# Performance work log

Measured on AMD Instinct MI355X. Metric: run time of the kernel, lower is better.

The kernel has to match this reference:

```python
import jax, jax.numpy as jnp
import numpy as np

B, S, D = 16, 256, 256      # batch, seq_len, input_size (= 2*hidden)
H = 128                     # hidden size per direction
NL = 2                      # num layers
A = 8                       # n_actions
DK = D // 4                 # attention projection dim = 64
SRU_IN = 2 * D              # cat(rnn_input, attn_pool) = 512


def setup_inputs() -> dict:
    key = jax.random.key(0)
    ks = jax.random.split(key, 12)
    stdv = 1.0 / np.sqrt(DK)
    inp = {
        "x": jax.random.normal(ks[0], (B, S, D), jnp.float32),
        "x_mask": jnp.zeros((B, S), bool),
        "actions": jax.random.randint(ks[1], (B,), 0, A),
        # SeqAttentionAction params (reset_parameters: uniform(-stdv,stdv), biases zero)
        "w1": jax.random.uniform(ks[2], (A, D, DK), jnp.float32, -stdv, stdv),
        "b1": jnp.zeros((A, DK), jnp.float32),
        "w2": jax.random.uniform(ks[3], (A, D, DK), jnp.float32, -stdv, stdv),
        "b2": jnp.zeros((A, DK), jnp.float32),
        "v": jax.random.uniform(ks[4], (A, DK), jnp.float32, -stdv, stdv),
        # SRU params: per layer, forward & backward cells. k=4 slices (x~, f, r, highway)
        "sru_w_f": jax.random.uniform(ks[5], (NL, SRU_IN, 4 * H), jnp.float32, -0.05, 0.05),
        "sru_b_f": jnp.zeros((NL, 2 * H), jnp.float32),
        "sru_w_b": jax.random.uniform(ks[6], (NL, SRU_IN, 4 * H), jnp.float32, -0.05, 0.05),
        "sru_b_b": jnp.zeros((NL, 2 * H), jnp.float32),
    }
    return inp


def _sru_layer(X, W, b):
    """SRU (use_tanh=1). X:(S,B,Din) -> (S,B,H)."""
    U = jnp.einsum("sbd,dk->sbk", X, W)           # (S,B,4H)
    u0, uf, ur, hw = jnp.split(U, 4, axis=-1)
    bf, br = jnp.split(b, 2)
    f = jax.nn.sigmoid(uf + bf)
    r = jax.nn.sigmoid(ur + br)

    def step(c, t):
        f_t, u_t, r_t, hw_t = t
        c = f_t * c + (1.0 - f_t) * u_t
        h = r_t * jnp.tanh(c) + (1.0 - r_t) * hw_t
        return c, h

    c0 = jnp.zeros((X.shape[1], f.shape[-1]), X.dtype)
    _, hs = jax.lax.scan(step, c0, (f, u0, r, hw))
    return hs


def _attn_pools(memory, rnn_input, x_mask, w1a, b1a, w2a, b2a, va):
    """Action-conditioned tanh attention, vectorized over all timesteps.
    memory:(B,L,D) rnn_input:(S,B,D) -> pools:(S,B,D) (detached, as in torch .data)."""
    xt = jnp.einsum("bld,bdk->blk", memory, w1a) + b1a[:, None]    # (B,L,K)
    yt = jnp.einsum("sbd,bdk->sbk", rnn_input, w2a) + b2a[None]    # (S,B,K)
    t = jnp.tanh(xt[None] + yt[:, :, None])                        # (S,B,L,K)
    scores = jnp.einsum("sblk,bk->sbl", t, va)                     # (S,B,L)
    scores = jnp.where(x_mask[None], -jnp.inf, scores)
    att = jax.nn.softmax(scores, axis=-1)
    pools = jnp.einsum("sbl,bld->sbd", att, memory)
    return jax.lax.stop_gradient(pools)


def reference(x, x_mask, actions, w1, b1, w2, b2, v,
              sru_w_f, sru_b_f, sru_w_b, sru_b_b):
    memory = x                                # (B,L,D)
    out = jnp.transpose(x, (1, 0, 2))         # (S,B,D)
    # one-hot matmul selection == gather by action index
    w1a, b1a = w1[actions], b1[actions]
    w2a, b2a = w2[actions], b2[actions]
    va = v[actions]
    for i in range(NL):
        pools = _attn_pools(memory, out, x_mask, w1a, b1a, w2a, b2a, va)
        inputs = jnp.concatenate([out, pools], axis=2)   # (S,B,2D); inputs_f == inputs_b
        hf = _sru_layer(inputs, sru_w_f[i], sru_b_f[i])
        hb = _sru_layer(inputs, sru_w_b[i], sru_b_b[i])
        out = jnp.concatenate([hf, hb], axis=2)          # (S,B,2H)=(S,B,D)
    return jnp.transpose(out, (1, 0, 2))                 # (B,S,D)
```

## Files before the change

kernel.cpp:

```cpp
#include <hip/hip_runtime.h>
#include <hip/hip_bf16.h>

#define S_ 256
#define D_ 256
#define K_ 64
#define SIN 512
#define F4H 512

typedef unsigned short u16;
typedef __attribute__((ext_vector_type(8))) short short8;
typedef __attribute__((ext_vector_type(4))) float f32x4;

__device__ __forceinline__ float rcpf(float x) { return __builtin_amdgcn_rcpf(x); }
__device__ __forceinline__ float fast_sigmoid(float x) {
  return rcpf(1.0f + __expf(-x));
}
__device__ __forceinline__ float fast_tanh(float x) {
  return 1.0f - 2.0f * rcpf(__expf(2.0f * x) + 1.0f);
}
__device__ __forceinline__ u16 f2bf(float f) {
  unsigned int u = __float_as_uint(f);
  return (u16)((u + 0x7fff + ((u >> 16) & 1)) >> 16);
}

__global__ __launch_bounds__(256) void k_prep(const float* __restrict__ sw_f,
    const float* __restrict__ sw_b, u16* __restrict__ wt,
    const float* __restrict__ x, u16* __restrict__ xT,
    const int* __restrict__ araw, int* __restrict__ act_out,
    int* __restrict__ status) {
  if (blockIdx.x == 0 && blockIdx.y == 0 && blockIdx.z == 0 && threadIdx.x == 0) {
    bool oddzero = true;
    for (int i = 1; i < 16; i += 2) oddzero = oddzero && (araw[i] == 0);
    bool ok = true;
    for (int b = 0; b < 16; ++b) {
      int v = oddzero ? araw[2 * b] : araw[b];
      act_out[b] = (v < 0) ? 0 : (v > 7 ? 7 : v);
      ok = ok && (v >= 0 && v < 8);
    }
    *status = ok ? 1 : 0;
  }
  __shared__ u16 tile[64][66];
  int tj = threadIdx.x & 63, ti = threadIdx.x >> 6;
  int z = blockIdx.z;
  if (z < 4) {
    int layer = z >> 1;
    const float* src = (z & 1) ? sw_b : sw_f;
    int k0 = blockIdx.x * 64, n0 = blockIdx.y * 64;
#pragma unroll
    for (int i = ti; i < 64; i += 4)
      tile[i][tj] = f2bf(src[layer * 262144 + (k0 + i) * 512 + n0 + tj]);
    __syncthreads();
#pragma unroll
    for (int j = ti; j < 64; j += 4)
      wt[z * 262144 + (n0 + j) * 512 + k0 + tj] = tile[tj][j];
  } else {
    if (blockIdx.x >= 4 || blockIdx.y >= 4) return;
    int b = z - 4;
    int l0 = blockIdx.x * 64, d0 = blockIdx.y * 64;
#pragma unroll
    for (int i = ti; i < 64; i += 4)
      tile[i][tj] = f2bf(x[b * 65536 + (l0 + i) * 256 + d0 + tj]);
    __syncthreads();
#pragma unroll
    for (int j = ti; j < 64; j += 4)
      xT[b * 65536 + (d0 + j) * 256 + l0 + tj] = tile[tj][j];
  }
}

__global__ __launch_bounds__(256) void k_xt(const float* __restrict__ x,
    const int* __restrict__ act, const float* __restrict__ w1,
    const float* __restrict__ b1, float* __restrict__ xtT) {
  __shared__ float As[16][17], Bs[16][68];
  int b = blockIdx.y;
  int a = act[b];
  int l0 = blockIdx.x * 16;
  const float* A = x + b * (S_ * D_);
  const float* W = w1 + a * (D_ * K_);
  int tid = threadIdx.x;
  int ty = tid >> 4, tx = tid & 15;
  float acc[4] = {};
  for (int kk = 0; kk < D_; kk += 16) {
    As[ty][tx] = A[(l0 + ty) * D_ + kk + tx];
    *(float4*)&Bs[ty][tx << 2] = *(const float4*)(W + (kk + ty) * K_ + (tx << 2));
    __syncthreads();
#pragma unroll
    for (int k = 0; k < 16; ++k) {
      float av = As[ty][k];
      acc[0] += av * Bs[k][(tx << 2) + 0];
      acc[1] += av * Bs[k][(tx << 2) + 1];
      acc[2] += av * Bs[k][(tx << 2) + 2];
      acc[3] += av * Bs[k][(tx << 2) + 3];
    }
    __syncthreads();
  }
#pragma unroll
  for (int j = 0; j < 4; ++j) {
    int n = (tx << 2) + j;
    xtT[(b << 14) + n * 256 + l0 + ty] = acc[j] + b1[a * K_ + n];
  }
}

__global__ __launch_bounds__(256) void k_score(const float* __restrict__ xtT,
    const float* __restrict__ curb, int sstride, int bstride,
    const float* __restrict__ w2, const float* __restrict__ b2,
    const float* __restrict__ v, const int* __restrict__ act,
    const unsigned char* __restrict__ xmask, u16* __restrict__ scores) {
  __shared__ float yts[4][K_], vas[K_], curs[4][256];
  __shared__ float redm[4][4], reds[4][4];
  int tid = threadIdx.x;
  int bid = blockIdx.x;
  int b = bid & 15, s4 = bid >> 4;
  int a = act[b];
  if (tid < 64) vas[tid] = v[a * K_ + tid];
#pragma unroll
  for (int rr = 0; rr < 4; ++rr)
    curs[rr][tid] = curb[b * bstride + (s4 * 4 + rr) * sstride + tid];
  __syncthreads();
  {
    int r = tid >> 6, k = tid & 63;
    const float* wcol = w2 + a * (D_ * K_) + k;
    float accv = b2[a * K_ + k];
#pragma unroll 8
    for (int d = 0; d < 256; ++d) accv += curs[r][d] * wcol[d * K_];
    yts[r][k] = accv;
  }
  __syncthreads();
  float acc0 = 0.f, acc1 = 0.f, acc2 = 0.f, acc3 = 0.f;
  {
    const float* xb = xtT + (b << 14) + tid;
#pragma unroll
    for (int k = 0; k < 64; ++k) {
      float xv = xb[k * 256];
      float vv = vas[k];
      acc0 += vv * fast_tanh(xv + yts[0][k]);
      acc1 += vv * fast_tanh(xv + yts[1][k]);
      acc2 += vv * fast_tanh(xv + yts[2][k]);
      acc3 += vv * fast_tanh(xv + yts[3][k]);
    }
    if (xmask[b * S_ + tid]) { acc0 = acc1 = acc2 = acc3 = -1e30f; }
  }
  int wid = tid >> 6;
  float m0 = acc0, m1 = acc1, m2 = acc2, m3 = acc3;
#pragma unroll
  for (int d = 32; d; d >>= 1) {
    m0 = fmaxf(m0, __shfl_xor(m0, d));
    m1 = fmaxf(m1, __shfl_xor(m1, d));
    m2 = fmaxf(m2, __shfl_xor(m2, d));
    m3 = fmaxf(m3, __shfl_xor(m3, d));
  }
  if ((tid & 63) == 0) {
    redm[0][wid] = m0; redm[1][wid] = m1; redm[2][wid] = m2; redm[3][wid] = m3;
  }
  __syncthreads();
  m0 = fmaxf(fmaxf(redm[0][0], redm[0][1]), fmaxf(redm[0][2], redm[0][3]));
  m1 = fmaxf(fmaxf(redm[1][0], redm[1][1]), fmaxf(redm[1][2], redm[1][3]));
  m2 = fmaxf(fmaxf(redm[2][0], redm[2][1]), fmaxf(redm[2][2], redm[2][3]));
  m3 = fmaxf(fmaxf(redm[3][0], redm[3][1]), fmaxf(redm[3][2], redm[3][3]));
  float p0 = __expf(acc0 - m0), p1 = __expf(acc1 - m1);
  float p2 = __expf(acc2 - m2), p3 = __expf(acc3 - m3);
  float s0 = p0, s1 = p1, s2 = p2, s3 = p3;
#pragma unroll
  for (int d = 32; d; d >>= 1) {
    s0 += __shfl_xor(s0, d);
    s1 += __shfl_xor(s1, d);
    s2 += __shfl_xor(s2, d);
    s3 += __shfl_xor(s3, d);
  }
  if ((tid & 63) == 0) {
    reds[0][wid] = s0; reds[1][wid] = s1; reds[2][wid] = s2; reds[3][wid] = s3;
  }
  __syncthreads();
  s0 = reds[0][0] + reds[0][1] + reds[0][2] + reds[0][3];
  s1 = reds[1][0] + reds[1][1] + reds[1][2] + reds[1][3];
  s2 = reds[2][0] + reds[2][1] + reds[2][2] + reds[2][3];
  s3 = reds[3][0] + reds[3][1] + reds[3][2] + reds[3][3];
  u16* dst = scores + ((s4 * 4) * 16 + b) * 256 + tid;
  dst[0]        = f2bf(p0 * rcpf(s0));
  dst[16 * 256] = f2bf(p1 * rcpf(s1));
  dst[32 * 256] = f2bf(p2 * rcpf(s2));
  dst[48 * 256] = f2bf(p3 * rcpf(s3));
}

__global__ __launch_bounds__(256) void k_poolm(const u16* __restrict__ scores,
    const u16* __restrict__ xT, const float* __restrict__ curb,
    int sstride, int bstride, u16* __restrict__ inp) {
  __shared__ u16 As[128][72];
  __shared__ u16 Bs[128][72];
  int b = blockIdx.z;
  int m0 = blockIdx.x * 128, n0 = blockIdx.y * 128;
  int tid = threadIdx.x;
  int wid = tid >> 6, lane = tid & 63;
  int wm = wid >> 1, wn = wid & 1;
  f32x4 acc[4][4];
#pragma unroll
  for (int i = 0; i < 4; ++i)
#pragma unroll
    for (int j = 0; j < 4; ++j) acc[i][j] = (f32x4){0.f, 0.f, 0.f, 0.f};
  int srow = tid >> 1, shalf = tid & 1;
  int lrow = lane & 15, lk = (lane >> 4) << 3;
  for (int kk = 0; kk < 256; kk += 64) {
    const u16* ga = scores + ((m0 + srow) * 16 + b) * 256 + kk + shalf * 32;
    const u16* gb = xT + b * 65536 + (n0 + srow) * 256 + kk + shalf * 32;
#pragma unroll
    for (int j = 0; j < 4; ++j) {
      *(short8*)&As[srow][shalf * 32 + j * 8] = *(const short8*)(ga + j * 8);
      *(short8*)&Bs[srow][shalf * 32 + j * 8] = *(const short8*)(gb + j * 8);
    }
    __syncthreads();
#pragma unroll
    for (int ks = 0; ks < 2; ++ks) {
      short8 af[4], bf[4];
#pragma unroll
      for (int mi = 0; mi < 4; ++mi)
        af[mi] = *(const short8*)&As[wm * 64 + mi * 16 + lrow][ks * 32 + lk];
#pragma unroll
      for (int ni = 0; ni < 4; ++ni)
        bf[ni] = *(const short8*)&Bs[wn * 64 + ni * 16 + lrow][ks * 32 + lk];
#pragma unroll
      for (int mi = 0; mi < 4; ++mi)
#pragma unroll
        for (int ni = 0; ni < 4; ++ni)
          acc[mi][ni] = __builtin_amdgcn_mfma_f32_16x16x32_bf16(
              af[mi], bf[ni], acc[mi][ni], 0, 0, 0);
    }
    __syncthreads();
  }
#pragma unroll
  for (int mi = 0; mi < 4; ++mi)
#pragma unroll
    for (int ni = 0; ni < 4; ++ni) {
      int r0 = m0 + wm * 64 + mi * 16 + ((lane >> 4) << 2);
      int c = n0 + wn * 64 + ni * 16 + (lane & 15);
#pragma unroll
      for (int r = 0; r < 4; ++r)
        inp[((r0 + r) * 16 + b) * SIN + 256 + c] = f2bf(acc[mi][ni][r]);
    }
#pragma unroll
  for (int i = 0; i < 16; ++i) {
    int idx = i * 256 + tid;
    int so = idx >> 5, d4 = (idx & 31) << 2;
    float4 v4 = *(const float4*)(curb + b * bstride + (m0 + so) * sstride + n0 + d4);
    ushort4 o;
    o.x = f2bf(v4.x); o.y = f2bf(v4.y); o.z = f2bf(v4.z); o.w = f2bf(v4.w);
    *(ushort4*)(inp + ((m0 + so) * 16 + b) * SIN + n0 + d4) = o;
  }
}

__global__ __launch_bounds__(256) void k_mfma(const u16* __restrict__ inp,
    const u16* __restrict__ wt, float* __restrict__ Uf, float* __restrict__ Ub,
    int layer) {
  __shared__ u16 As[128][72];
  __shared__ u16 Bs[128][72];
  float* U = blockIdx.z ? Ub : Uf;
  const u16* W = wt + (layer * 2 + blockIdx.z) * 262144;
  int m0 = blockIdx.x * 128, n0 = blockIdx.y * 128;
  int tid = threadIdx.x;
  int wid = tid >> 6, lane = tid & 63;
  int wm = wid >> 1, wn = wid & 1;
  f32x4 acc[4][4];
#pragma unroll
  for (int i = 0; i < 4; ++i)
#pragma unroll
    for (int j = 0; j < 4; ++j) acc[i][j] = (f32x4){0.f, 0.f, 0.f, 0.f};
  int srow = tid >> 1, shalf = tid & 1;
  int lrow = lane & 15, lk = (lane >> 4) << 3;
  for (int kk = 0; kk < 512; kk += 64) {
    const u16* ga = inp + (m0 + srow) * SIN + kk + shalf * 32;
    const u16* gb = W + (n0 + srow) * 512 + kk + shalf * 32;
#pragma unroll
    for (int j = 0; j < 4; ++j) {
      *(short8*)&As[srow][shalf * 32 + j * 8] = *(const short8*)(ga + j * 8);
      *(short8*)&Bs[srow][shalf * 32 + j * 8] = *(const short8*)(gb + j * 8);
    }
    __syncthreads();
#pragma unroll
    for (int ks = 0; ks < 2; ++ks) {
      short8 af[4], bf[4];
#pragma unroll
      for (int mi = 0; mi < 4; ++mi)
        af[mi] = *(const short8*)&As[wm * 64 + mi * 16 + lrow][ks * 32 + lk];
#pragma unroll
      for (int ni = 0; ni < 4; ++ni)
        bf[ni] = *(const short8*)&Bs[wn * 64 + ni * 16 + lrow][ks * 32 + lk];
#pragma unroll
      for (int mi = 0; mi < 4; ++mi)
#pragma unroll
        for (int ni = 0; ni < 4; ++ni)
          acc[mi][ni] = __builtin_amdgcn_mfma_f32_16x16x32_bf16(
              af[mi], bf[ni], acc[mi][ni], 0, 0, 0);
    }
    __syncthreads();
  }
#pragma unroll
  for (int mi = 0; mi < 4; ++mi)
#pragma unroll
    for (int ni = 0; ni < 4; ++ni) {
      int r0 = m0 + wm * 64 + mi * 16 + ((lane >> 4) << 2);
      int c = n0 + wn * 64 + ni * 16 + (lane & 15);
#pragma unroll
      for (int r = 0; r < 4; ++r)
        U[(r0 + r) * F4H + c] = acc[mi][ni][r];
    }
}

__global__ __launch_bounds__(256) void k_scan(const float* __restrict__ Uf,
    const float* __restrict__ Ub, const float* __restrict__ bfp,
    const float* __restrict__ bbp, float* __restrict__ obase,
    int o_sstride, int o_bstride, const int* __restrict__ status, int final) {
  int tid = threadIdx.x;
  int chain = blockIdx.x * 16 + (tid >> 4);
  int lane = tid & 15;
  int dir = chain >> 11;
  int rem = chain & 2047;
  int b = rem >> 7, h = rem & 127;
  const float* U = dir ? Ub : Uf;
  const float* bias = dir ? bbp : bfp;
  float bfv = bias[h], brv = bias[128 + h];
  const float* up = U + b * 512 + h;
  float* op = obase + b * o_bstride + dir * 128 + h;
  int s0 = lane * 16;
  float fv[16], u0[16], rv[16], hw[16];
#pragma unroll
  for (int t = 0; t < 16; ++t) {
    const float* q = up + (s0 + t) * 8192;
    u0[t] = q[0]; fv[t] = q[128]; rv[t] = q[256]; hw[t] = q[384];
  }
  float A = 1.f, Bv = 0.f;
#pragma unroll
  for (int t = 0; t < 16; ++t) {
    float f = fast_sigmoid(fv[t] + bfv);
    fv[t] = f;
    Bv = f * Bv + (1.f - f) * u0[t];
    A = A * f;
  }
#pragma unroll
  for (int d = 1; d < 16; d <<= 1) {
    float Ap = __shfl_up(A, d, 16);
    float Bp = __shfl_up(Bv, d, 16);
    if (lane >= d) { Bv = A * Bp + Bv; A = A * Ap; }
  }
  float cin = __shfl_up(Bv, 1, 16);
  if (lane == 0) cin = 0.f;
  float c = cin;
  bool ok = final ? (*status != 0) : true;
#pragma unroll
  for (int t = 0; t < 16; ++t) {
    float f = fv[t];
    c = f * (c - u0[t]) + u0[t];
    float r = fast_sigmoid(rv[t] + brv);
    float hv = r * fast_tanh(c) + (1.f - r) * hw[t];
    op[(s0 + t) * o_sstride] = ok ? hv : 20.0f;
  }
}

__global__ __launch_bounds__(256) void k_fill(float* out, float v, int n) {
  int idx = blockIdx.x * 256 + threadIdx.x;
  if (idx < n) out[idx] = v;
}

extern "C" void kernel_launch(void* const* d_in, const int* in_sizes, int n_in,
                              void* d_out, int out_size, void* d_ws, size_t ws_size,
                              hipStream_t stream) {
  float* out = (float*)d_out;
  int fill_grid = (out_size + 255) / 256;

  const int exp_sizes[12] = {1048576, 4096, 16, 131072, 512, 131072, 512, 512,
                             524288, 512, 524288, 512};
  bool env_ok = (n_in == 12);
  if (env_ok)
    for (int i = 0; i < 12; ++i) env_ok = env_ok && (in_sizes[i] == exp_sizes[i]);
  if (!env_ok) {
    k_fill<<<fill_grid, 256, 0, stream>>>(out, 10.0f, out_size);
    return;
  }

  const float* x    = (const float*)d_in[0];
  const unsigned char* xmask = (const unsigned char*)d_in[1];
  const float* w1   = (const float*)d_in[3];
  const float* b1   = (const float*)d_in[4];
  const float* w2   = (const float*)d_in[5];
  const float* b2   = (const float*)d_in[6];
  const float* v    = (const float*)d_in[7];
  const float* sw_f = (const float*)d_in[8];
  const float* sb_f = (const float*)d_in[9];
  const float* sw_b = (const float*)d_in[10];
  const float* sb_b = (const float*)d_in[11];

  float* ws = (float*)d_ws;
  size_t off = 0;
  float* pb0    = ws + off; off += 1048576;
  float* xtT    = ws + off; off += 262144;
  float* Uf     = ws + off; off += 2097152;
  float* Ub     = ws + off; off += 2097152;
  u16*   scores = (u16*)(ws + off); off += 524288;
  u16*   xT     = (u16*)(ws + off); off += 524288;
  u16*   inp    = (u16*)(ws + off); off += 1048576;
  u16*   wt     = (u16*)(ws + off); off += 524288;
  int*   act    = (int*)(ws + off); off += 16;
  int*   status = (int*)(ws + off); off += 16;

  if (ws_size < off * sizeof(float)) {
    k_fill<<<fill_grid, 256, 0, stream>>>(out, 30.0f, out_size);
    return;
  }

  k_prep<<<dim3(8, 8, 20), 256, 0, stream>>>(sw_f, sw_b, wt, x, xT,
      (const int*)d_in[2], act, status);
  k_xt<<<dim3(16, 16), 256, 0, stream>>>(x, act, w1, b1, xtT);

  for (int layer = 0; layer < 2; ++layer) {
    const float* curb = layer ? pb0 : x;
    int sstride = layer ? 4096 : 256;
    int bstride = layer ? 256 : 65536;
    float* nxt      = layer ? out : pb0;
    int o_sstride   = layer ? 256 : 4096;
    int o_bstride   = layer ? 65536 : 256;
    k_score<<<1024, 256, 0, stream>>>(xtT, curb, sstride, bstride, w2, b2, v,
                                      act, xmask, scores);
    k_poolm<<<dim3(2, 2, 16), 256, 0, stream>>>(scores, xT, curb, sstride,
                                                bstride, inp);
    k_mfma<<<dim3(32, 4, 2), 256, 0, stream>>>(inp, wt, Uf, Ub, layer);
    k_scan<<<256, 256, 0, stream>>>(Uf, Ub, sb_f + layer * 256, sb_b + layer * 256,
                                    nxt, o_sstride, o_bstride, status, layer);
  }
}
```

Before: 166.2 us.

## Split yt projection into tiled kernel, shrink pool tiles, stage scan output via LDS

Moves the per-timestep w2 projection out of k_score into a separate shared-memory tiled GEMM kernel, so w2 columns are no longer reloaded per block with strided access. It also halves the k_poolm tile to 64x64 so the grid grows from 64 to 256 blocks, and stages k_scan outputs in LDS so global writes are coalesced along h instead of strided. The cost is one extra kernel launch per layer and an extra workspace buffer round-trip.

Result: faster. 156.4 us (-5.9%).

```diff
diff --git a/kernel.cpp b/kernel.cpp
--- a/kernel.cpp
+++ b/kernel.cpp
@@ -100,29 +100,55 @@
   }
 }
 
+__global__ __launch_bounds__(256) void k_yt(const float* __restrict__ curb,
+    int sstride, int bstride, const int* __restrict__ act,
+    const float* __restrict__ w2, const float* __restrict__ b2,
+    float* __restrict__ yt) {
+  __shared__ float As[16][17], Bs[16][68];
+  int b = blockIdx.y;
+  int a = act[b];
+  int s0 = blockIdx.x * 16;
+  const float* A = curb + b * bstride;
+  const float* W = w2 + a * (D_ * K_);
+  int tid = threadIdx.x;
+  int ty = tid >> 4, tx = tid & 15;
+  float acc[4] = {};
+  for (int kk = 0; kk < D_; kk += 16) {
+    As[ty][tx] = A[(s0 + ty) * sstride + kk + tx];
+    *(float4*)&Bs[ty][tx << 2] = *(const float4*)(W + (kk + ty) * K_ + (tx << 2));
+    __syncthreads();
+#pragma unroll
+    for (int k = 0; k < 16; ++k) {
+      float av = As[ty][k];
+      acc[0] += av * Bs[k][(tx << 2) + 0];
+      acc[1] += av * Bs[k][(tx << 2) + 1];
+      acc[2] += av * Bs[k][(tx << 2) + 2];
+      acc[3] += av * Bs[k][(tx << 2) + 3];
+    }
+    __syncthreads();
+  }
+  float4 o;
+  o.x = acc[0] + b2[a * K_ + (tx << 2) + 0];
+  o.y = acc[1] + b2[a * K_ + (tx << 2) + 1];
+  o.z = acc[2] + b2[a * K_ + (tx << 2) + 2];
+  o.w = acc[3] + b2[a * K_ + (tx << 2) + 3];
+  *(float4*)(yt + ((s0 + ty) * 16 + b) * K_ + (tx << 2)) = o;
+}
+
 __global__ __launch_bounds__(256) void k_score(const float* __restrict__ xtT,
-    const float* __restrict__ curb, int sstride, int bstride,
-    const float* __restrict__ w2, const float* __restrict__ b2,
-    const float* __restrict__ v, const int* __restrict__ act,
-    const unsigned char* __restrict__ xmask, u16* __restrict__ scores) {
-  __shared__ float yts[4][K_], vas[K_], curs[4][256];
+    const float* __restrict__ yt, const float* __restrict__ v,
+    const int* __restrict__ act, const unsigned char* __restrict__ xmask,
+    u16* __restrict__ scores) {
+  __shared__ float yts[4][K_], vas[K_];
   __shared__ float redm[4][4], reds[4][4];
   int tid = threadIdx.x;
   int bid = blockIdx.x;
   int b = bid & 15, s4 = bid >> 4;
   int a = act[b];
   if (tid < 64) vas[tid] = v[a * K_ + tid];
-#pragma unroll
-  for (int rr = 0; rr < 4; ++rr)
-    curs[rr][tid] = curb[b * bstride + (s4 * 4 + rr) * sstride + tid];
-  __syncthreads();
   {
-    int r = tid >> 6, k = tid & 63;
-    const float* wcol = w2 + a * (D_ * K_) + k;
-    float accv = b2[a * K_ + k];
-#pragma unroll 8
-    for (int d = 0; d < 256; ++d) accv += curs[r][d] * wcol[d * K_];
-    yts[r][k] = accv;
+    int row = tid >> 6, k = tid & 63;
+    yts[row][k] = yt[((s4 * 4 + row) * 16 + b) * K_ + k];
   }
   __syncthreads();
   float acc0 = 0.f, acc1 = 0.f, acc2 = 0.f, acc3 = 0.f;
@@ -184,61 +210,60 @@
 __global__ __launch_bounds__(256) void k_poolm(const u16* __restrict__ scores,
     const u16* __restrict__ xT, const float* __restrict__ curb,
     int sstride, int bstride, u16* __restrict__ inp) {
-  __shared__ u16 As[128][72];
-  __shared__ u16 Bs[128][72];
+  __shared__ u16 As[64][72];
+  __shared__ u16 Bs[64][72];
   int b = blockIdx.z;
-  int m0 = blockIdx.x * 128, n0 = blockIdx.y * 128;
+  int m0 = blockIdx.x * 64, n0 = blockIdx.y * 64;
   int tid = threadIdx.x;
   int wid = tid >> 6, lane = tid & 63;
   int wm = wid >> 1, wn = wid & 1;
-  f32x4 acc[4][4];
-#pragma unroll
-  for (int i = 0; i < 4; ++i)
-#pragma unroll
-    for (int j = 0; j < 4; ++j) acc[i][j] = (f32x4){0.f, 0.f, 0.f, 0.f};
-  int srow = tid >> 1, shalf = tid & 1;
+  f32x4 acc[2][2];
+#pragma unroll
+  for (int i = 0; i < 2; ++i)
+#pragma unroll
+    for (int j = 0; j < 2; ++j) acc[i][j] = (f32x4){0.f, 0.f, 0.f, 0.f};
+  int srow = tid >> 2, soff = (tid & 3) * 16;
   int lrow = lane & 15, lk = (lane >> 4) << 3;
   for (int kk = 0; kk < 256; kk += 64) {
-    const u16* ga = scores + ((m0 + srow) * 16 + b) * 256 + kk + shalf * 32;
-    const u16* gb = xT + b * 65536 + (n0 + srow) * 256 + kk + shalf * 32;
-#pragma unroll
-    for (int j = 0; j < 4; ++j) {
-      *(short8*)&As[srow][shalf * 32 + j * 8] = *(const short8*)(ga + j * 8);
-      *(short8*)&Bs[srow][shalf * 32 + j * 8] = *(const short8*)(gb + j * 8);
-    }
+    const u16* ga = scores + ((m0 + srow) * 16 + b) * 256 + kk + soff;
+    const u16* gb = xT + b * 65536 + (n0 + srow) * 256 + kk + soff;
+    *(short8*)&As[srow][soff]     = *(const short8*)(ga);
+    *(short8*)&As[srow][soff + 8] = *(const short8*)(ga + 8);
+    *(short8*)&Bs[srow][soff]     = *(const short8*)(gb);
+    *(short8*)&Bs[srow][soff + 8] = *(const short8*)(gb + 8);
     __syncthreads();
 #pragma unroll
     for (int ks = 0; ks < 2; ++ks) {
-      short8 af[4], bf[4];
-#pragma unroll
-      for (int mi = 0; mi < 4; ++mi)
-        af[mi] = *(const short8*)&As[wm * 64 + mi * 16 + lrow][ks * 32 + lk];
-#pragma unroll
-      for (int ni = 0; ni < 4; ++ni)
-        bf[ni] = *(const short8*)&Bs[wn * 64 + ni * 16 + lrow][ks * 32 + lk];
-#pragma unroll
-      for (int mi = 0; mi < 4; ++mi)
-#pragma unroll
-        for (int ni = 0; ni < 4; ++ni)
+      short8 af[2], bf[2];
+#pragma unroll
+      for (int mi = 0; mi < 2; ++mi)
+        af[mi] = *(const short8*)&As[wm * 32 + mi * 16 + lrow][ks * 32 + lk];
+#pragma unroll
+      for (int ni = 0; ni < 2; ++ni)
+        bf[ni] = *(const short8*)&Bs[wn * 32 + ni * 16 + lrow][ks * 32 + lk];
+#pragma unroll
+      for (int mi = 0; mi < 2; ++mi)
+#pragma unroll
+        for (int ni = 0; ni < 2; ++ni)
           acc[mi][ni] = __builtin_amdgcn_mfma_f32_16x16x32_bf16(
               af[mi], bf[ni], acc[mi][ni], 0, 0, 0);
     }
     __syncthreads();
   }
 #pragma unroll
-  for (int mi = 0; mi < 4; ++mi)
-#pragma unroll
-    for (int ni = 0; ni < 4; ++ni) {
-      int r0 = m0 + wm * 64 + mi * 16 + ((lane >> 4) << 2);
-      int c = n0 + wn * 64 + ni * 16 + (lane & 15);
+  for (int mi = 0; mi < 2; ++mi)
+#pragma unroll
+    for (int ni = 0; ni < 2; ++ni) {
+      int r0 = m0 + wm * 32 + mi * 16 + ((lane >> 4) << 2);
+      int c = n0 + wn * 32 + ni * 16 + (lane & 15);
 #pragma unroll
       for (int r = 0; r < 4; ++r)
         inp[((r0 + r) * 16 + b) * SIN + 256 + c] = f2bf(acc[mi][ni][r]);
     }
 #pragma unroll
-  for (int i = 0; i < 16; ++i) {
+  for (int i = 0; i < 4; ++i) {
     int idx = i * 256 + tid;
-    int so = idx >> 5, d4 = (idx & 31) << 2;
+    int so = idx >> 4, d4 = (idx & 15) << 2;
     float4 v4 = *(const float4*)(curb + b * bstride + (m0 + so) * sstride + n0 + d4);
     ushort4 o;
     o.x = f2bf(v4.x); o.y = f2bf(v4.y); o.z = f2bf(v4.z); o.w = f2bf(v4.w);
@@ -307,8 +332,10 @@
     const float* __restrict__ Ub, const float* __restrict__ bfp,
     const float* __restrict__ bbp, float* __restrict__ obase,
     int o_sstride, int o_bstride, const int* __restrict__ status, int final) {
-  int tid = threadIdx.x;
-  int chain = blockIdx.x * 16 + (tid >> 4);
+  __shared__ float so[16][257];
+  int tid = threadIdx.x;
+  int cloc = tid >> 4;
+  int chain = blockIdx.x * 16 + cloc;
   int lane = tid & 15;
   int dir = chain >> 11;
   int rem = chain & 2047;
@@ -317,7 +344,6 @@
   const float* bias = dir ? bbp : bfp;
   float bfv = bias[h], brv = bias[128 + h];
   const float* up = U + b * 512 + h;
-  float* op = obase + b * o_bstride + dir * 128 + h;
   int s0 = lane * 16;
   float fv[16], u0[16], rv[16], hw[16];
 #pragma unroll
@@ -342,14 +368,25 @@
   float cin = __shfl_up(Bv, 1, 16);
   if (lane == 0) cin = 0.f;
   float c = cin;
-  bool ok = final ? (*status != 0) : true;
 #pragma unroll
   for (int t = 0; t < 16; ++t) {
     float f = fv[t];
     c = f * (c - u0[t]) + u0[t];
     float r = fast_sigmoid(rv[t] + brv);
-    float hv = r * fast_tanh(c) + (1.f - r) * hw[t];
-    op[(s0 + t) * o_sstride] = ok ? hv : 20.0f;
+    so[cloc][s0 + t] = r * fast_tanh(c) + (1.f - r) * hw[t];
+  }
+  __syncthreads();
+  bool ok = final ? (*status != 0) : true;
+  int h_idx = tid & 15, s_idx = tid >> 4;
+  int c2 = blockIdx.x * 16 + h_idx;
+  int dir2 = c2 >> 11, rem2 = c2 & 2047;
+  int b2 = rem2 >> 7, h2 = rem2 & 127;
+  float* op2 = obase + b2 * o_bstride + dir2 * 128 + h2;
+#pragma unroll
+  for (int j = 0; j < 16; ++j) {
+    int s = s_idx * 16 + j;
+    float hv = so[h_idx][s];
+    op2[s * o_sstride] = ok ? hv : 20.0f;
   }
 }
 
@@ -390,6 +427,7 @@
   size_t off = 0;
   float* pb0    = ws + off; off += 1048576;
   float* xtT    = ws + off; off += 262144;
+  float* yt     = ws + off; off += 262144;
   float* Uf     = ws + off; off += 2097152;
   float* Ub     = ws + off; off += 2097152;
   u16*   scores = (u16*)(ws + off); off += 524288;
@@ -415,9 +453,9 @@
     float* nxt      = layer ? out : pb0;
     int o_sstride   = layer ? 256 : 4096;
     int o_bstride   = layer ? 65536 : 256;
-    k_score<<<1024, 256, 0, stream>>>(xtT, curb, sstride, bstride, w2, b2, v,
-                                      act, xmask, scores);
-    k_poolm<<<dim3(2, 2, 16), 256, 0, stream>>>(scores, xT, curb, sstride,
+    k_yt<<<dim3(16, 16), 256, 0, stream>>>(curb, sstride, bstride, act, w2, b2, yt);
+    k_score<<<1024, 256, 0, stream>>>(xtT, yt, v, act, xmask, scores);
+    k_poolm<<<dim3(4, 4, 16), 256, 0, stream>>>(scores, xT, curb, sstride,
                                                 bstride, inp);
     k_mfma<<<dim3(32, 4, 2), 256, 0, stream>>>(inp, wt, Uf, Ub, layer);
     k_scan<<<256, 256, 0, stream>>>(Uf, Ub, sb_f + layer * 256, sb_b + layer * 256,
```
